# Kernel tuning notes

Measured on AMD Instinct MI355X. Metric: run time of the kernel, lower is better.

The kernel has to match this reference:

```python
import jax, jax.numpy as jnp
import numpy as np

B, S, H, D = 2, 2048, 16, 64
DIM = H * D          # 1024, fused QKV dense outputs 3*DIM
EPS = 1e-6
NINF = -10000.0      # additive mask value from module
STD = 0.02           # truncated-normal init stddev (plain normal here)


def setup_inputs() -> dict:
    key = jax.random.key(0)
    k0, k1, k2 = jax.random.split(key, 3)
    x = jax.random.normal(k0, (B, S, DIM), jnp.float32)
    ln_g = jnp.ones((DIM,), jnp.float32)
    ln_b = jnp.zeros((DIM,), jnp.float32)
    wqkv = jax.random.normal(k1, (DIM, 3 * DIM), jnp.float32) * STD
    bqkv = jnp.zeros((3 * DIM,), jnp.float32)
    wo = jax.random.normal(k2, (DIM, DIM), jnp.float32) * STD
    bo = jnp.zeros((DIM,), jnp.float32)
    return {"x": x, "ln_g": ln_g, "ln_b": ln_b, "wqkv": wqkv,
            "bqkv": bqkv, "wo": wo, "bo": bo}


def reference(x, ln_g, ln_b, wqkv, bqkv, wo, bo):
    b, s, _ = x.shape
    # pre-norm LayerNorm (axis=-1, eps=1e-6)
    mu = jnp.mean(x, axis=-1, keepdims=True)
    var = jnp.mean(jnp.square(x - mu), axis=-1, keepdims=True)
    h = (x - mu) * jax.lax.rsqrt(var + EPS) * ln_g + ln_b
    # fused QKV projection, split along feature axis
    qkv = h @ wqkv + bqkv                       # [b, s, 3*DIM]
    q, k, v = jnp.split(qkv, 3, axis=2)

    def heads(t):                               # [b, s, DIM] -> [b, H, s, D]
        return t.reshape(b, s, H, D).transpose(0, 2, 1, 3)

    q, k, v = heads(q), heads(k), heads(v)
    scores = jnp.einsum("bhqd,bhkd->bhqk", q, k) / jnp.sqrt(jnp.float32(D))
    # causal mask: positions j > i get ninf (mask=None path, Lq == Lk)
    causal = (jnp.arange(s)[:, None] < jnp.arange(s)[None, :]).astype(jnp.float32) * NINF
    a = jax.nn.softmax(scores + causal, axis=-1)  # attdrop rate 0 -> identity
    ctx = jnp.einsum("bhqk,bhkd->bhqd", a, v)
    ctx = ctx.transpose(0, 2, 1, 3).reshape(b, s, DIM)
    # output dense + residual (drop rate 0 -> identity)
    return x + ctx @ wo + bo
```

## Files before the change

kernel.cpp:

```cpp
#include <hip/hip_runtime.h>
#include <hip/hip_bf16.h>

#define B_   2
#define S_   2048
#define H_   16
#define D_   64
#define DIM_ 1024
#define QKV_SZ (32 * 2048 * 64)

typedef __attribute__((ext_vector_type(8))) short bf16x8;
typedef __attribute__((ext_vector_type(4))) float f32x4;
typedef unsigned short u16;
typedef unsigned int u32;

static __device__ __forceinline__ u16 f2bf(float f) {
    union { float f; unsigned u; } v; v.f = f;
    unsigned u = v.u;
    unsigned r = (u + 0x7fffu + ((u >> 16) & 1u)) >> 16;
    return (u16)r;
}
static __device__ __forceinline__ float exp2_fast(float x) {
    float r; asm("v_exp_f32 %0, %1" : "=v"(r) : "v"(x)); return r;
}
static __device__ __forceinline__ u32 cvtpk_bf16(float lo, float hi) {
    u32 r; asm("v_cvt_pk_bf16_f32 %0, %1, %2" : "=v"(r) : "v"(lo), "v"(hi)); return r;
}
static __device__ __forceinline__ void gload_lds16(const u16* g, u16* l) {
    __builtin_amdgcn_global_load_lds(
        (const __attribute__((address_space(1))) void*)g,
        (__attribute__((address_space(3))) void*)l, 16, 0, 0);
}

__global__ __launch_bounds__(256) void prep_kernel(
    const float* __restrict__ x, const float* __restrict__ g,
    const float* __restrict__ b, u16* __restrict__ hb,
    const float* __restrict__ wqkv, u16* __restrict__ wqkvT,
    const float* __restrict__ wo, u16* __restrict__ woT)
{
    __shared__ u16 T[64][65];
    __shared__ float rs[4], rss[4];
    int bid = blockIdx.x;
    int t = threadIdx.x;
    if (bid < 4096) {
        int row = bid;
        const float4 v = ((const float4*)(x + row * DIM_))[t];
        float s  = v.x + v.y + v.z + v.w;
        float ss = v.x*v.x + v.y*v.y + v.z*v.z + v.w*v.w;
#pragma unroll
        for (int m = 1; m < 64; m <<= 1) { s += __shfl_xor(s, m); ss += __shfl_xor(ss, m); }
        int wid = t >> 6, lane = t & 63;
        if (lane == 0) { rs[wid] = s; rss[wid] = ss; }
        __syncthreads();
        s  = rs[0] + rs[1] + rs[2] + rs[3];
        ss = rss[0] + rss[1] + rss[2] + rss[3];
        float mu   = s * (1.0f / DIM_);
        float var  = ss * (1.0f / DIM_) - mu * mu;
        float rstd = rsqrtf(var + 1e-6f);
        const float4 gv = ((const float4*)g)[t];
        const float4 bv = ((const float4*)b)[t];
        ushort4 ov;
        ov.x = f2bf((v.x - mu) * rstd * gv.x + bv.x);
        ov.y = f2bf((v.y - mu) * rstd * gv.y + bv.y);
        ov.z = f2bf((v.z - mu) * rstd * gv.z + bv.z);
        ov.w = f2bf((v.w - mu) * rstd * gv.w + bv.w);
        ((ushort4*)(hb + row * DIM_))[t] = ov;
    } else {
        const float* src; u16* dst; int R, C, c0, r0;
        if (bid < 4864) {
            int idx = bid - 4096;
            src = wqkv; dst = wqkvT; R = 1024; C = 3072;
            c0 = (idx % 48) * 64; r0 = (idx / 48) * 64;
        } else {
            int idx = bid - 4864;
            src = wo; dst = woT; R = 1024; C = 1024;
            c0 = (idx % 16) * 64; r0 = (idx / 16) * 64;
        }
        int rl = t >> 4, cl = (t & 15) * 4;
#pragma unroll
        for (int p = 0; p < 4; p++) {
            float4 v = *(const float4*)(src + (size_t)(r0 + rl + p * 16) * C + c0 + cl);
            T[cl + 0][rl + p * 16] = f2bf(v.x);
            T[cl + 1][rl + p * 16] = f2bf(v.y);
            T[cl + 2][rl + p * 16] = f2bf(v.z);
            T[cl + 3][rl + p * 16] = f2bf(v.w);
        }
        __syncthreads();
#pragma unroll
        for (int p = 0; p < 4; p++) {
            ushort4 o;
            o.x = T[rl + p * 16][cl + 0];
            o.y = T[rl + p * 16][cl + 1];
            o.z = T[rl + p * 16][cl + 2];
            o.w = T[rl + p * 16][cl + 3];
            *(ushort4*)(dst + (size_t)(c0 + rl + p * 16) * R + r0 + cl) = o;
        }
    }
}

__global__ __launch_bounds__(256) void qkv_gemm128(
    const u16* __restrict__ A, const u16* __restrict__ Bw,
    const float* __restrict__ bias, u16* __restrict__ qkv)
{
    __shared__ __align__(16) u16 As[2][128 * 32];
    __shared__ __align__(16) u16 Bs[2][128 * 32];
    int t = threadIdx.x;
    int bn = blockIdx.x * 128, bm = blockIdx.y * 128;
    int wid = t >> 6, lane = t & 63;
    int wm = wid >> 1, wn = wid & 1;
    int l15 = lane & 15, l4 = lane >> 4;

    f32x4 zero = {0.f, 0.f, 0.f, 0.f};
    f32x4 acc[4][4];
#pragma unroll
    for (int i = 0; i < 4; i++)
#pragma unroll
        for (int j = 0; j < 4; j++) acc[i][j] = zero;

    int scol = ((lane & 3) ^ ((lane >> 3) & 3)) * 8;
    const u16* aSrc = A  + (size_t)(bm + wid * 32 + (lane >> 2)) * 1024 + scol;
    const u16* bSrc = Bw + (size_t)(bn + wid * 32 + (lane >> 2)) * 1024 + scol;
    int rdk = ((l15 >> 1) & 3) << 4;

#define STAGE_G(bufsel, kk) do { \
        char* Ad = (char*)As + (bufsel) * 8192 + wid * 2048; \
        char* Bd = (char*)Bs + (bufsel) * 8192 + wid * 2048; \
        gload_lds16(aSrc + (kk),             (u16*)Ad); \
        gload_lds16(aSrc + (kk) + 16 * 1024, (u16*)(Ad + 1024)); \
        gload_lds16(bSrc + (kk),             (u16*)Bd); \
        gload_lds16(bSrc + (kk) + 16 * 1024, (u16*)(Bd + 1024)); \
    } while (0)

    STAGE_G(0, 0);
    __syncthreads();
    int cur = 0;
    for (int kt = 0; kt < 32; ++kt) {
        if (kt < 31) STAGE_G(cur ^ 1, (kt + 1) * 32);
        const char* Ab = (const char*)As + cur * 8192;
        const char* Bb = (const char*)Bs + cur * 8192;
        bf16x8 af[4], bf[4];
#pragma unroll
        for (int mi = 0; mi < 4; mi++)
            af[mi] = *(const bf16x8*)(Ab + (wm * 64 + mi * 16 + l15) * 64 + (l4 * 16 ^ rdk));
#pragma unroll
        for (int ni = 0; ni < 4; ni++)
            bf[ni] = *(const bf16x8*)(Bb + (wn * 64 + ni * 16 + l15) * 64 + (l4 * 16 ^ rdk));
        __builtin_amdgcn_s_setprio(1);
#pragma unroll
        for (int mi = 0; mi < 4; mi++)
#pragma unroll
            for (int ni = 0; ni < 4; ni++)
                acc[mi][ni] = __builtin_amdgcn_mfma_f32_16x16x32_bf16(af[mi], bf[ni], acc[mi][ni], 0, 0, 0);
        __builtin_amdgcn_s_setprio(0);
        __syncthreads();
        cur ^= 1;
    }
#pragma unroll
    for (int mi = 0; mi < 4; mi++)
#pragma unroll
        for (int ni = 0; ni < 4; ni++) {
            int col = bn + wn * 64 + ni * 16 + l15;
            int which = col >> 10, f = col & 1023;
            int hh = f >> 6, d = f & 63;
            float bs = bias[col];
            if (which == 2) {
                int s_base = bm + wm * 64 + mi * 16 + l4 * 4;
                int bb = s_base >> 11, s = s_base & 2047;
                ushort4 pk;
                pk.x = f2bf(acc[mi][ni][0] + bs);
                pk.y = f2bf(acc[mi][ni][1] + bs);
                pk.z = f2bf(acc[mi][ni][2] + bs);
                pk.w = f2bf(acc[mi][ni][3] + bs);
                *(ushort4*)(qkv + (size_t)2 * QKV_SZ +
                            ((size_t)(bb * 16 + hh) * 64 + d) * 2048 + s) = pk;
            } else {
                float scl = (which == 0) ? 0.18033688011112042f : 1.0f;
#pragma unroll
                for (int r = 0; r < 4; r++) {
                    int row = bm + wm * 64 + mi * 16 + l4 * 4 + r;
                    int bb = row >> 11, s = row & 2047;
                    qkv[(size_t)which * QKV_SZ + ((size_t)(bb * 16 + hh) * 2048 + s) * 64 + d] =
                        f2bf((acc[mi][ni][r] + bs) * scl);
                }
            }
        }
}

__global__ __launch_bounds__(256) void out_gemm128(
    const u16* __restrict__ A, const u16* __restrict__ Bw,
    const float* __restrict__ bias, const float* __restrict__ xres,
    float* __restrict__ out)
{
    __shared__ __align__(16) u16 As[2][128 * 32];
    __shared__ __align__(16) u16 Bs[2][64 * 32];
    int t = threadIdx.x;
    int bn = blockIdx.x * 64, bm = blockIdx.y * 128;
    int wid = t >> 6, lane = t & 63;
    int l15 = lane & 15, l4 = lane >> 4;

    f32x4 zero = {0.f, 0.f, 0.f, 0.f};
    f32x4 acc[2][4];
#pragma unroll
    for (int i = 0; i < 2; i++)
#pragma unroll
        for (int j = 0; j < 4; j++) acc[i][j] = zero;

    int scol = ((t & 3) ^ ((t >> 3) & 3)) * 8;
    const u16* aSrc = A  + (size_t)(bm + (t >> 2)) * 1024 + scol;
    const u16* bSrc = Bw + (size_t)(bn + (t >> 2)) * 1024 + scol;
    int rdk = ((l15 >> 1) & 3) << 4;

#define OSTG(bufsel, kk) do { \
        char* Ad = (char*)As + (bufsel) * 8192 + wid * 1024; \
        char* Bd = (char*)Bs + (bufsel) * 4096 + wid * 1024; \
        gload_lds16(aSrc + (kk),             (u16*)Ad); \
        gload_lds16(aSrc + (kk) + 64 * 1024, (u16*)(Ad + 4096)); \
        gload_lds16(bSrc + (kk),             (u16*)Bd); \
    } while (0)

    OSTG(0, 0);
    __syncthreads();
    int cur = 0;
    for (int kt = 0; kt < 32; ++kt) {
        if (kt < 31) OSTG(cur ^ 1, (kt + 1) * 32);
        const char* Ab = (const char*)As + cur * 8192;
        const char* Bb = (const char*)Bs + cur * 4096;
        bf16x8 af[2], bf[4];
#pragma unroll
        for (int mi = 0; mi < 2; mi++)
            af[mi] = *(const bf16x8*)(Ab + (wid * 32 + mi * 16 + l15) * 64 + (l4 * 16 ^ rdk));
#pragma unroll
        for (int ni = 0; ni < 4; ni++)
            bf[ni] = *(const bf16x8*)(Bb + (ni * 16 + l15) * 64 + (l4 * 16 ^ rdk));
        __builtin_amdgcn_s_setprio(1);
#pragma unroll
        for (int mi = 0; mi < 2; mi++)
#pragma unroll
            for (int ni = 0; ni < 4; ni++)
                acc[mi][ni] = __builtin_amdgcn_mfma_f32_16x16x32_bf16(af[mi], bf[ni], acc[mi][ni], 0, 0, 0);
        __builtin_amdgcn_s_setprio(0);
        __syncthreads();
        cur ^= 1;
    }
#pragma unroll
    for (int mi = 0; mi < 2; mi++)
#pragma unroll
        for (int ni = 0; ni < 4; ni++) {
            int col = bn + ni * 16 + l15;
            float bs = bias[col];
#pragma unroll
            for (int r = 0; r < 4; r++) {
                int row = bm + wid * 32 + mi * 16 + l4 * 4 + r;
                out[(size_t)row * 1024 + col] = xres[(size_t)row * 1024 + col] + acc[mi][ni][r] + bs;
            }
        }
}

__global__ __launch_bounds__(256) void attn_kernel(
    const u16* __restrict__ qbuf, const u16* __restrict__ kbuf,
    const u16* __restrict__ vbuf, u16* __restrict__ ctx)
{
    __shared__ __align__(16) char Ks[64 * 128];
    __shared__ __align__(16) char Vt[64 * 128];
    __shared__ __align__(16) char Pb[4 * 16 * 128];

    int t = threadIdx.x, wid = t >> 6, lane = t & 63;
    int l15 = lane & 15, l4 = lane >> 4;
    int idx = blockIdx.x;
    int qt = 31 - (idx >> 5);
    int bh = idx & 31;
    int q0 = qt * 64;
    int sr = t >> 3, g = t & 7;
    int bb = bh >> 4, hh = bh & 15;
    f32x4 zero = {0.f, 0.f, 0.f, 0.f};

    const u16* Q = qbuf + (size_t)(bh * 2048 + q0 + wid * 16) * 64;
    bf16x8 aq0 = *(const bf16x8*)(Q + l15 * 64 + 8 * l4);
    bf16x8 aq1 = *(const bf16x8*)(Q + l15 * 64 + 32 + 8 * l4);

    f32x4 o[4];
#pragma unroll
    for (int f = 0; f < 4; f++) o[f] = zero;
    float m_run = -1e30f;
    float l_run = 0.f;

    int kswz = (16 * g) ^ ((sr & 7) << 4);
    char* Pw = Pb + wid * 2048;
    int prow = l15 * 128;
    int pkey = (l15 & 7) << 4;
    int qloc = wid * 16 + l15;

    const u16* Kbase = kbuf + (size_t)bh * 2048 * 64;
    const u16* Vbase = vbuf + (size_t)bh * 64 * 2048;

    bf16x8 ck0 = *(const bf16x8*)(Kbase + (size_t)sr * 64 + g * 8);
    bf16x8 ck1 = *(const bf16x8*)(Kbase + (size_t)(sr + 32) * 64 + g * 8);
    bf16x8 cv0 = *(const bf16x8*)(Vbase + (size_t)sr * 2048 + g * 8);
    bf16x8 cv1 = *(const bf16x8*)(Vbase + (size_t)(sr + 32) * 2048 + g * 8);

    for (int kt = 0; kt <= qt; ++kt) {
        *(bf16x8*)(Ks + sr * 128 + kswz) = ck0;
        *(bf16x8*)(Ks + (sr + 32) * 128 + kswz) = ck1;
        *(bf16x8*)(Vt + sr * 128 + kswz) = cv0;
        *(bf16x8*)(Vt + (sr + 32) * 128 + kswz) = cv1;
        {
            int nkt = (kt < qt) ? kt + 1 : qt;
            const u16* Kn = Kbase + (size_t)nkt * 64 * 64;
            const u16* Vn = Vbase + (size_t)nkt * 64;
            bf16x8 a = *(const bf16x8*)(Kn + (size_t)sr * 64 + g * 8);
            bf16x8 b = *(const bf16x8*)(Kn + (size_t)(sr + 32) * 64 + g * 8);
            bf16x8 c = *(const bf16x8*)(Vn + (size_t)sr * 2048 + g * 8);
            bf16x8 d = *(const bf16x8*)(Vn + (size_t)(sr + 32) * 2048 + g * 8);
            __syncthreads();

            f32x4 sc[4];
            __builtin_amdgcn_s_setprio(1);
#pragma unroll
            for (int nf = 0; nf < 4; ++nf) {
                int krow = nf * 16 + l15;
                int kkey = (krow & 7) << 4;
                bf16x8 kb0 = *(const bf16x8*)(Ks + krow * 128 + ((16 * l4) ^ kkey));
                bf16x8 kb1 = *(const bf16x8*)(Ks + krow * 128 + ((64 + 16 * l4) ^ kkey));
                f32x4 z = zero;
                z = __builtin_amdgcn_mfma_f32_16x16x32_bf16(kb0, aq0, z, 0, 0, 0);
                z = __builtin_amdgcn_mfma_f32_16x16x32_bf16(kb1, aq1, z, 0, 0, 0);
                sc[nf] = z;
            }
            __builtin_amdgcn_s_setprio(0);

            if (kt == qt) {
#pragma unroll
                for (int nf = 0; nf < 4; nf++)
#pragma unroll
                    for (int r = 0; r < 4; r++) {
                        int ka = nf * 16 + 4 * l4 + r;
                        if (ka > qloc) sc[nf][r] = -1e30f;
                    }
            }
            float lmax = sc[0][0];
#pragma unroll
            for (int nf = 0; nf < 4; nf++)
#pragma unroll
                for (int r = 0; r < 4; r++) lmax = fmaxf(lmax, sc[nf][r]);
            if (__any(lmax > m_run + 10.f)) {
                float m0 = lmax;
                m0 = fmaxf(m0, __shfl_xor(m0, 16));
                m0 = fmaxf(m0, __shfl_xor(m0, 32));
                float mn = fmaxf(m_run, m0);
                float al = exp2_fast(m_run - mn);
                l_run *= al;
                m_run = mn;
                float a0 = __shfl(al, 4 * l4 + 0);
                float a1 = __shfl(al, 4 * l4 + 1);
                float a2 = __shfl(al, 4 * l4 + 2);
                float a3 = __shfl(al, 4 * l4 + 3);
#pragma unroll
                for (int f = 0; f < 4; f++) {
                    o[f][0] *= a0; o[f][1] *= a1; o[f][2] *= a2; o[f][3] *= a3;
                }
            }
            float psum = 0.f;
#pragma unroll
            for (int nf = 0; nf < 4; nf++)
#pragma unroll
                for (int r = 0; r < 4; r++) {
                    float pv = exp2_fast(sc[nf][r] - m_run);
                    sc[nf][r] = pv; psum += pv;
                }
            l_run += psum;
#pragma unroll
            for (int nf = 0; nf < 4; nf++) {
                uint2 w;
                w.x = cvtpk_bf16(sc[nf][0], sc[nf][1]);
                w.y = cvtpk_bf16(sc[nf][2], sc[nf][3]);
                *(uint2*)(Pw + prow + ((nf * 32 + l4 * 8) ^ pkey)) = w;
            }
            __builtin_amdgcn_s_setprio(1);
#pragma unroll
            for (int kk = 0; kk < 2; kk++) {
                bf16x8 pa = *(const bf16x8*)(Pw + prow + ((64 * kk + 16 * l4) ^ pkey));
#pragma unroll
                for (int f = 0; f < 4; f++) {
                    int vrow = f * 16 + l15;
                    int vkey = (vrow & 7) << 4;
                    bf16x8 vb = *(const bf16x8*)(Vt + vrow * 128 + ((64 * kk + 16 * l4) ^ vkey));
                    o[f] = __builtin_amdgcn_mfma_f32_16x16x32_bf16(pa, vb, o[f], 0, 0, 0);
                }
            }
            __builtin_amdgcn_s_setprio(0);
            __syncthreads();
            ck0 = a; ck1 = b; cv0 = c; cv1 = d;
        }
    }
    l_run += __shfl_xor(l_run, 16);
    l_run += __shfl_xor(l_run, 32);
#pragma unroll
    for (int r = 0; r < 4; r++) {
        float lr = __shfl(l_run, 4 * l4 + r);
        float inv = 1.f / lr;
        int qa = q0 + wid * 16 + l4 * 4 + r;
        u16* dst = ctx + (size_t)(bb * 2048 + qa) * 1024 + hh * 64;
#pragma unroll
        for (int f = 0; f < 4; f++) dst[f * 16 + l15] = f2bf(o[f][r] * inv);
    }
}

extern "C" void kernel_launch(void* const* d_in, const int* in_sizes, int n_in,
                              void* d_out, int out_size, void* d_ws, size_t ws_size,
                              hipStream_t stream)
{
    const float* x    = (const float*)d_in[0];
    const float* ln_g = (const float*)d_in[1];
    const float* ln_b = (const float*)d_in[2];
    const float* wqkv = (const float*)d_in[3];
    const float* bqkv = (const float*)d_in[4];
    const float* wo   = (const float*)d_in[5];
    const float* bo   = (const float*)d_in[6];
    float* out = (float*)d_out;

    char* ws = (char*)d_ws;
    u16* hbuf  = (u16*)ws;
    u16* qkvb  = (u16*)(ws + 8388608);
    u16* ctxb  = (u16*)(ws + 33554432);
    u16* wqkvT = ctxb;
    u16* woT   = (u16*)(ws + 41943040);

    prep_kernel<<<5120, 256, 0, stream>>>(x, ln_g, ln_b, hbuf, wqkv, wqkvT, wo, woT);
    qkv_gemm128<<<dim3(24, 32), 256, 0, stream>>>(hbuf, wqkvT, bqkv, qkvb);
    attn_kernel<<<1024, 256, 0, stream>>>(
        qkvb, qkvb + QKV_SZ, qkvb + 2 * QKV_SZ, ctxb);
    out_gemm128<<<dim3(16, 32), 256, 0, stream>>>(ctxb, woT, bo, x, out);
}
```

Measured before the change: 114.6 us.

## Split long causal attention rows across two blocks and merge partial softmax results

The causal attention kernel's longest query tiles (qt 17-31) are each split into two blocks that process half of the key tiles. Each half writes unnormalized bf16 partial outputs plus running max and sum, and a new merge kernel rescales and combines them into ctx. This is meant to balance the triangular workload and cut the tail of the attention grid. The cost is an extra launch, extra global traffic for the partials, and additional bf16 rounding of the intermediates.

Result: slower. 122.3 us (+6.8%).

```diff
diff --git a/kernel.cpp b/kernel.cpp
--- a/kernel.cpp
+++ b/kernel.cpp
@@ -18,6 +18,9 @@
     unsigned u = v.u;
     unsigned r = (u + 0x7fffu + ((u >> 16) & 1u)) >> 16;
     return (u16)r;
+}
+static __device__ __forceinline__ float bf2f(u16 x) {
+    union { unsigned u; float f; } v; v.u = ((u32)x) << 16; return v.f;
 }
 static __device__ __forceinline__ float exp2_fast(float x) {
     float r; asm("v_exp_f32 %0, %1" : "=v"(r) : "v"(x)); return r;
@@ -257,7 +260,8 @@
 
 __global__ __launch_bounds__(256) void attn_kernel(
     const u16* __restrict__ qbuf, const u16* __restrict__ kbuf,
-    const u16* __restrict__ vbuf, u16* __restrict__ ctx)
+    const u16* __restrict__ vbuf, u16* __restrict__ ctx,
+    u16* __restrict__ po, float* __restrict__ pml)
 {
     __shared__ __align__(16) char Ks[64 * 128];
     __shared__ __align__(16) char Vt[64 * 128];
@@ -265,9 +269,22 @@
 
     int t = threadIdx.x, wid = t >> 6, lane = t & 63;
     int l15 = lane & 15, l4 = lane >> 4;
-    int idx = blockIdx.x;
-    int qt = 31 - (idx >> 5);
-    int bh = idx & 31;
+    int bid = blockIdx.x;
+    int qt, bh, ktB, ktE, pair = 0, half = 0;
+    bool split;
+    if (bid < 960) {
+        split = true;
+        pair = bid >> 1; half = bid & 1;
+        qt = 31 - (pair >> 5); bh = pair & 31;
+        int h = (qt + 1) >> 1;
+        if (half == 0) { ktB = 0; ktE = h - 1; }
+        else           { ktB = h; ktE = qt;   }
+    } else {
+        split = false;
+        int u = bid - 960;
+        qt = 16 - (u >> 5); bh = u & 31;
+        ktB = 0; ktE = qt;
+    }
     int q0 = qt * 64;
     int sr = t >> 3, g = t & 7;
     int bb = bh >> 4, hh = bh & 15;
@@ -292,18 +309,18 @@
     const u16* Kbase = kbuf + (size_t)bh * 2048 * 64;
     const u16* Vbase = vbuf + (size_t)bh * 64 * 2048;
 
-    bf16x8 ck0 = *(const bf16x8*)(Kbase + (size_t)sr * 64 + g * 8);
-    bf16x8 ck1 = *(const bf16x8*)(Kbase + (size_t)(sr + 32) * 64 + g * 8);
-    bf16x8 cv0 = *(const bf16x8*)(Vbase + (size_t)sr * 2048 + g * 8);
-    bf16x8 cv1 = *(const bf16x8*)(Vbase + (size_t)(sr + 32) * 2048 + g * 8);
-
-    for (int kt = 0; kt <= qt; ++kt) {
+    bf16x8 ck0 = *(const bf16x8*)(Kbase + (size_t)(ktB * 64 + sr) * 64 + g * 8);
+    bf16x8 ck1 = *(const bf16x8*)(Kbase + (size_t)(ktB * 64 + sr + 32) * 64 + g * 8);
+    bf16x8 cv0 = *(const bf16x8*)(Vbase + (size_t)sr * 2048 + ktB * 64 + g * 8);
+    bf16x8 cv1 = *(const bf16x8*)(Vbase + (size_t)(sr + 32) * 2048 + ktB * 64 + g * 8);
+
+    for (int kt = ktB; kt <= ktE; ++kt) {
         *(bf16x8*)(Ks + sr * 128 + kswz) = ck0;
         *(bf16x8*)(Ks + (sr + 32) * 128 + kswz) = ck1;
         *(bf16x8*)(Vt + sr * 128 + kswz) = cv0;
         *(bf16x8*)(Vt + (sr + 32) * 128 + kswz) = cv1;
         {
-            int nkt = (kt < qt) ? kt + 1 : qt;
+            int nkt = (kt < ktE) ? kt + 1 : ktE;
             const u16* Kn = Kbase + (size_t)nkt * 64 * 64;
             const u16* Vn = Vbase + (size_t)nkt * 64;
             bf16x8 a = *(const bf16x8*)(Kn + (size_t)sr * 64 + g * 8);
@@ -393,14 +410,68 @@
     }
     l_run += __shfl_xor(l_run, 16);
     l_run += __shfl_xor(l_run, 32);
-#pragma unroll
-    for (int r = 0; r < 4; r++) {
-        float lr = __shfl(l_run, 4 * l4 + r);
-        float inv = 1.f / lr;
-        int qa = q0 + wid * 16 + l4 * 4 + r;
-        u16* dst = ctx + (size_t)(bb * 2048 + qa) * 1024 + hh * 64;
-#pragma unroll
-        for (int f = 0; f < 4; f++) dst[f * 16 + l15] = f2bf(o[f][r] * inv);
+    if (!split) {
+#pragma unroll
+        for (int r = 0; r < 4; r++) {
+            float lr = __shfl(l_run, 4 * l4 + r);
+            float inv = 1.f / lr;
+            int qa = q0 + wid * 16 + l4 * 4 + r;
+            u16* dst = ctx + (size_t)(bb * 2048 + qa) * 1024 + hh * 64;
+#pragma unroll
+            for (int f = 0; f < 4; f++) dst[f * 16 + l15] = f2bf(o[f][r] * inv);
+        }
+    } else {
+        size_t pbase = (size_t)(pair * 2 + half) * 64;
+#pragma unroll
+        for (int r = 0; r < 4; r++) {
+            int q = wid * 16 + l4 * 4 + r;
+            u16* dst = po + (pbase + q) * 64;
+#pragma unroll
+            for (int f = 0; f < 4; f++) dst[f * 16 + l15] = f2bf(o[f][r]);
+        }
+        if (l4 == 0) {
+            int q = wid * 16 + l15;
+            pml[(pbase + q) * 2 + 0] = m_run;
+            pml[(pbase + q) * 2 + 1] = l_run;
+        }
+    }
+}
+
+__global__ __launch_bounds__(256) void merge_kernel(
+    const u16* __restrict__ po, const float* __restrict__ pml,
+    u16* __restrict__ ctx)
+{
+    int pair = blockIdx.x;
+    int qt = 31 - (pair >> 5), bh = pair & 31;
+    int t = threadIdx.x;
+    int q = t >> 2, dg = (t & 3) * 16;
+    size_t baseA = (size_t)(pair * 2 + 0) * 64 + q;
+    size_t baseB = (size_t)(pair * 2 + 1) * 64 + q;
+    float mA = pml[baseA * 2], lA = pml[baseA * 2 + 1];
+    float mB = pml[baseB * 2], lB = pml[baseB * 2 + 1];
+    float m  = fmaxf(mA, mB);
+    float aA = exp2_fast(mA - m), aB = exp2_fast(mB - m);
+    float inv = 1.f / (lA * aA + lB * aB);
+    const u16* oA = po + baseA * 64 + dg;
+    const u16* oB = po + baseB * 64 + dg;
+    int bb = bh >> 4, hh = bh & 15;
+    int qa = qt * 64 + q;
+    u16* dst = ctx + (size_t)(bb * 2048 + qa) * 1024 + hh * 64 + dg;
+#pragma unroll
+    for (int c = 0; c < 2; c++) {
+        bf16x8 va = *(const bf16x8*)(oA + c * 8);
+        bf16x8 vb = *(const bf16x8*)(oB + c * 8);
+        ushort4 w0, w1;
+        w0.x = f2bf((bf2f((u16)va[0]) * aA + bf2f((u16)vb[0]) * aB) * inv);
+        w0.y = f2bf((bf2f((u16)va[1]) * aA + bf2f((u16)vb[1]) * aB) * inv);
+        w0.z = f2bf((bf2f((u16)va[2]) * aA + bf2f((u16)vb[2]) * aB) * inv);
+        w0.w = f2bf((bf2f((u16)va[3]) * aA + bf2f((u16)vb[3]) * aB) * inv);
+        w1.x = f2bf((bf2f((u16)va[4]) * aA + bf2f((u16)vb[4]) * aB) * inv);
+        w1.y = f2bf((bf2f((u16)va[5]) * aA + bf2f((u16)vb[5]) * aB) * inv);
+        w1.z = f2bf((bf2f((u16)va[6]) * aA + bf2f((u16)vb[6]) * aB) * inv);
+        w1.w = f2bf((bf2f((u16)va[7]) * aA + bf2f((u16)vb[7]) * aB) * inv);
+        *(ushort4*)(dst + c * 8)     = w0;
+        *(ushort4*)(dst + c * 8 + 4) = w1;
     }
 }
 
@@ -423,10 +494,13 @@
     u16* ctxb  = (u16*)(ws + 33554432);
     u16* wqkvT = ctxb;
     u16* woT   = (u16*)(ws + 41943040);
+    u16* po    = (u16*)ws;
+    float* pml = (float*)(ws + 7864320);
 
     prep_kernel<<<5120, 256, 0, stream>>>(x, ln_g, ln_b, hbuf, wqkv, wqkvT, wo, woT);
     qkv_gemm128<<<dim3(24, 32), 256, 0, stream>>>(hbuf, wqkvT, bqkv, qkvb);
-    attn_kernel<<<1024, 256, 0, stream>>>(
-        qkvb, qkvb + QKV_SZ, qkvb + 2 * QKV_SZ, ctxb);
+    attn_kernel<<<1504, 256, 0, stream>>>(
+        qkvb, qkvb + QKV_SZ, qkvb + 2 * QKV_SZ, ctxb, po, pml);
+    merge_kernel<<<480, 256, 0, stream>>>(po, pml, ctxb);
     out_gemm128<<<dim3(16, 32), 256, 0, stream>>>(ctxb, woT, bo, x, out);
 }
```
